# Performance work log

Hardware: AMD Instinct MI355X
Metric: run time of the kernel (lower is better)

The kernel has to match this reference:

```python
import jax, jax.numpy as jnp
import numpy as np

B, T, D, H = 2, 2048, 1024, 16  # batch, seq, hidden, heads; head_dim = 64


def setup_inputs() -> dict:
    key = jax.random.key(0)
    k1, k2, k3 = jax.random.split(key, 3)
    X = jax.random.normal(k1, (B, T, D), dtype=jnp.float32)
    # Dense(3*hidden_dim, use_bias=False): kernel [D, 3D]
    Wqkv = jax.random.normal(k2, (D, 3 * D), dtype=jnp.float32) / np.float32(np.sqrt(D))
    # Dense(hidden_dim, use_bias=False): kernel [D, D]
    Wproj = jax.random.normal(k3, (D, D), dtype=jnp.float32) / np.float32(np.sqrt(D))
    return {"X": X, "Wqkv": Wqkv, "Wproj": Wproj, "train": 0}


def reference(X, Wqkv, Wproj, train):
    # train=0 -> dropout is identity; the chunked online-softmax in the
    # original is mathematically exact softmax causal attention.
    b, t, d = X.shape
    hd = d // H
    qkv = X @ Wqkv                      # [B,T,3D]
    q, k, v = jnp.split(qkv, 3, axis=-1)
    q = q.reshape(b, t, H, hd)
    k = k.reshape(b, t, H, hd)
    v = v.reshape(b, t, H, hd)
    scale = 1.0 / jnp.sqrt(jnp.asarray(hd, dtype=X.dtype))
    scores = jnp.einsum('bqhd,bkhd->bhqk', q * scale, k)  # [B,H,T,T]
    causal = jnp.tril(jnp.ones((t, t), dtype=bool))
    scores = jnp.where(causal[None, None, :, :], scores, -jnp.inf)
    attn = jax.nn.softmax(scores, axis=-1)
    out = jnp.einsum('bhqk,bkhd->bqhd', attn, v).reshape(b, t, d)
    return out @ Wproj
```

## Files before the change

kernel.cpp:

```cpp
#include <hip/hip_runtime.h>


using u16 = unsigned short;
using u32 = unsigned int;

typedef __bf16 bf16x8 __attribute__((ext_vector_type(8)));
typedef __bf16 bf16x2 __attribute__((ext_vector_type(2)));
typedef float f32x4 __attribute__((ext_vector_type(4)));

#define DEV __device__ __forceinline__

DEV u16 f2bf(float f) { __bf16 h = (__bf16)f; return *(u16*)&h; }

DEV float bf2f(u16 v) {
  union { u32 u; float f; } x; x.u = (u32)v << 16; return x.f;
}

DEV u32 pk2(float lo, float hi) {
  bf16x2 t = {(__bf16)lo, (__bf16)hi};
  return *(u32*)&t;
}

DEV f32x4 mfma16(bf16x8 a, bf16x8 b, f32x4 c) {
  return __builtin_amdgcn_mfma_f32_16x16x32_bf16(a, b, c, 0, 0, 0);
}

DEV void gload_lds16(const void* g, void* l) {
  __builtin_amdgcn_global_load_lds(
      (const __attribute__((address_space(1))) void*)g,
      (__attribute__((address_space(3))) void*)l, 16, 0, 0);
}

DEV bf16x8 ld16(const u16* p) { return *(const bf16x8*)p; }

DEV void BAR() {
  __builtin_amdgcn_s_barrier();
  __builtin_amdgcn_sched_barrier(0);
}

DEV int vperm(int slot) {
  return ((((slot >> 4) & 2) | ((slot >> 2) & 1)) << 4) + (((slot >> 3) & 3) << 2) + (slot & 3);
}
DEV int vperm_inv(int k) {
  return (k & 0x23) | ((k & 0x10) >> 2) | ((k & 0x0c) << 1);
}


__global__ __launch_bounds__(256) void prep_kernel(
    const float* __restrict__ X, u16* __restrict__ Xb,
    const float* __restrict__ Wqkv, u16* __restrict__ Wqkvt,
    const float* __restrict__ Wproj, u16* __restrict__ Wprojt) {
  const int bid = blockIdx.x;
  const int t = threadIdx.x;

  if (bid < 2048) {
    int i = (bid * 256 + t) * 8;
    float4 a = *(const float4*)&X[i];
    float4 b = *(const float4*)&X[i + 4];
    union { u16 u[8]; uint4 v; } o;
    o.u[0] = f2bf(a.x); o.u[1] = f2bf(a.y); o.u[2] = f2bf(a.z); o.u[3] = f2bf(a.w);
    o.u[4] = f2bf(b.x); o.u[5] = f2bf(b.y); o.u[6] = f2bf(b.z); o.u[7] = f2bf(b.w);
    *(uint4*)&Xb[i] = o.v;
    return;
  }

  __shared__ float tile[64][65];
  const float* W; u16* Wt; int C, tb;
  if (bid < 2816) { W = Wqkv;  Wt = Wqkvt;  C = 3072; tb = bid - 2048; }
  else            { W = Wproj; Wt = Wprojt; C = 1024; tb = bid - 2816; }
  const int tilesC = C >> 6;
  const int tr = tb / tilesC, tc = tb % tilesC;
#pragma unroll
  for (int j = 0; j < 16; ++j) {
    int idx = j * 256 + t;
    int r = idx >> 6, c = idx & 63;
    tile[r][c] = W[(tr * 64 + r) * C + tc * 64 + c];
  }
  __syncthreads();
#pragma unroll
  for (int j = 0; j < 16; ++j) {
    int idx = j * 256 + t;
    int r = idx >> 6, c = idx & 63;
    Wt[(tc * 64 + r) * 1024 + tr * 64 + c] = f2bf(tile[c][r]);
  }
}


__global__ __launch_bounds__(512, 2) void gemm256_qkv_kernel(
    const u16* __restrict__ A, const u16* __restrict__ Bt,
    u16* __restrict__ Qb, u16* __restrict__ Kb, u16* __restrict__ VtP) {
  int bid = blockIdx.x;
  int bid2 = (bid & 7) * 32 + (bid >> 3);
  const int mt = bid2 >> 4, nt = bid2 & 15;
  const int m0 = mt * 256, n0 = nt * 192;
  const int tid = threadIdx.x;
  const int wid = tid >> 6, lane = tid & 63;
  const int g = lane >> 4, li = lane & 15;
  const int wm = wid >> 2, wn = wid & 3;

  __shared__ __align__(16) u16 lds[57344];

  const int srow = lane >> 3;
  const int scol = ((lane & 7) * 8) ^ ((srow & 7) << 3);

  auto ISSUE_A = [&](int s, int kt) {
    const int p = kt & 1;
#pragma unroll
    for (int is2 = 0; is2 < 2; ++is2) {
      int row = is2 * 64 + wid * 8 + srow;
      gload_lds16(&A[(size_t)(m0 + s * 128 + row) * 1024 + kt * 64 + scol],
                  &lds[s * 16384 + p * 8192 + is2 * 4096 + wid * 512]);
    }
  };
  auto ISSUE_B = [&](int kt) {
    const int p = kt & 1;
#pragma unroll
    for (int j = 0; j < 3; ++j) {
      int chunk = wid * 3 + j;
      int row = chunk * 8 + srow;
      gload_lds16(&Bt[(size_t)(n0 + row) * 1024 + kt * 64 + scol],
                  &lds[32768 + p * 12288 + chunk * 512]);
    }
  };

  auto LDA = [&](int p, int ks, bf16x8* aF) {
#pragma unroll
    for (int mi = 0; mi < 8; ++mi) {
      int row = mi * 16 + li;
      aF[mi] = ld16(&lds[wm * 16384 + p * 8192 + row * 64 +
                         ((ks * 32 + g * 8) ^ ((li & 7) << 3))]);
    }
  };
  auto LDB = [&](int p, int ks, bf16x8* bF) {
#pragma unroll
    for (int ni = 0; ni < 3; ++ni) {
      int row = wn * 48 + ni * 16 + li;
      bF[ni] = ld16(&lds[32768 + p * 12288 + row * 64 +
                         ((ks * 32 + g * 8) ^ ((li & 7) << 3))]);
    }
  };

  f32x4 acc[8][3] = {};
  bf16x8 a0[8], a1[8], bF[3];

  ISSUE_A(0, 0); ISSUE_A(1, 0); ISSUE_B(0);
  ISSUE_A(0, 1); ISSUE_A(1, 1);
  asm volatile("s_waitcnt vmcnt(4)" ::: "memory");
  BAR();

  for (int t = 0; t < 16; ++t) {
    const int p = t & 1;
    LDB(p, 0, bF);
    LDA(p, 0, a0);
    if (t + 1 < 16) ISSUE_B(t + 1);
    BAR();
    __builtin_amdgcn_s_setprio(1);
#pragma unroll
    for (int mi = 0; mi < 4; ++mi)
#pragma unroll
      for (int ni = 0; ni < 3; ++ni)
        acc[mi][ni] = mfma16(a0[mi], bF[ni], acc[mi][ni]);
    __builtin_amdgcn_s_setprio(0);
    BAR();
    LDA(p, 1, a1);
    BAR();
    __builtin_amdgcn_s_setprio(1);
#pragma unroll
    for (int mi = 4; mi < 8; ++mi)
#pragma unroll
      for (int ni = 0; ni < 3; ++ni)
        acc[mi][ni] = mfma16(a0[mi], bF[ni], acc[mi][ni]);
    __builtin_amdgcn_s_setprio(0);
    BAR();
    LDB(p, 1, bF);
    BAR();
    __builtin_amdgcn_s_setprio(1);
#pragma unroll
    for (int mi = 0; mi < 4; ++mi)
#pragma unroll
      for (int ni = 0; ni < 3; ++ni)
        acc[mi][ni] = mfma16(a1[mi], bF[ni], acc[mi][ni]);
    __builtin_amdgcn_s_setprio(0);
    BAR();
    if (t + 2 < 16) { ISSUE_A(0, t + 2); ISSUE_A(1, t + 2); }
    BAR();
    __builtin_amdgcn_s_setprio(1);
#pragma unroll
    for (int mi = 4; mi < 8; ++mi)
#pragma unroll
      for (int ni = 0; ni < 3; ++ni)
        acc[mi][ni] = mfma16(a1[mi], bF[ni], acc[mi][ni]);
    __builtin_amdgcn_s_setprio(0);
    if (t + 2 < 16) {
      asm volatile("s_waitcnt vmcnt(4)" ::: "memory");
    } else {
      asm volatile("s_waitcnt vmcnt(0)" ::: "memory");
    }
    BAR();
  }

#pragma unroll
  for (int mi = 0; mi < 8; ++mi)
#pragma unroll
    for (int ni = 0; ni < 3; ++ni) {
      int cc = n0 + wn * 48 + ni * 16 + li;
      int which = cc >> 10, rem = cc & 1023;
      int h = rem >> 6, dd = rem & 63;
      int rbase = m0 + wm * 128 + mi * 16 + g * 4;
      int bb = rbase >> 11, tt = rbase & 2047;
      if (which == 2) {
        int slot0 = (tt & ~63) + vperm_inv(tt & 63);
        size_t di = ((size_t)(bb * 16 + h) * 64 + dd) * 2048 + slot0;
        uint2 wv;
        wv.x = pk2(acc[mi][ni][0], acc[mi][ni][1]);
        wv.y = pk2(acc[mi][ni][2], acc[mi][ni][3]);
        *(uint2*)&VtP[di] = wv;
      } else {
        u16* dst = which == 0 ? Qb : Kb;
        float sc = which == 0 ? 0.18033688f : 1.0f;
        size_t di = ((size_t)(bb * 16 + h) * 2048 + tt) * 64 + dd;
#pragma unroll
        for (int r = 0; r < 4; ++r) dst[di + (size_t)r * 64] = f2bf(acc[mi][ni][r] * sc);
      }
    }
}


__global__ __launch_bounds__(256) void gemm_proj_kernel(
    const u16* __restrict__ A, const u16* __restrict__ Bt, float* __restrict__ OF) {
  int bid = blockIdx.x;
  int bid2 = (bid & 7) * 64 + (bid >> 3);
  const int mt = bid2 >> 3, nt = bid2 & 7;
  const int m0 = mt * 64, n0 = nt * 128;
  const int tid = threadIdx.x;
  const int wid = tid >> 6, lane = tid & 63;
  const int g = lane >> 4, li = lane & 15;
  const int wn = wid;

  __shared__ __align__(16) u16 As[2][64 * 64];
  __shared__ __align__(16) u16 Bs[2][128 * 64];

  f32x4 acc[4][2] = {};

  auto ISSUE = [&](int buf, int kt) {
#pragma unroll
    for (int iss = 0; iss < 2; ++iss) {
      int e = iss * 2048 + wid * 512 + lane * 8;
      int row = e >> 6;
      int kk = (e & 63) ^ ((row & 7) << 3);
      gload_lds16(&A[(size_t)(m0 + row) * 1024 + kt * 64 + kk], &As[buf][iss * 2048 + wid * 512]);
    }
#pragma unroll
    for (int iss = 0; iss < 4; ++iss) {
      int e = iss * 2048 + wid * 512 + lane * 8;
      int row = e >> 6;
      int kk = (e & 63) ^ ((row & 7) << 3);
      gload_lds16(&Bt[(size_t)(n0 + row) * 1024 + kt * 64 + kk], &Bs[buf][iss * 2048 + wid * 512]);
    }
  };

  ISSUE(0, 0);
  __syncthreads();
  int cur = 0;

  for (int kt = 0; kt < 16; ++kt) {
    if (kt + 1 < 16) ISSUE(cur ^ 1, kt + 1);
#pragma unroll
    for (int ks = 0; ks < 2; ++ks) {
      bf16x8 af[4], bfr[2];
#pragma unroll
      for (int mi = 0; mi < 4; ++mi)
        af[mi] = ld16(&As[cur][(mi * 16 + li) * 64 +
                               ((ks * 32 + g * 8) ^ ((li & 7) << 3))]);
#pragma unroll
      for (int ni = 0; ni < 2; ++ni)
        bfr[ni] = ld16(&Bs[cur][(wn * 32 + ni * 16 + li) * 64 +
                                ((ks * 32 + g * 8) ^ ((li & 7) << 3))]);
#pragma unroll
      for (int mi = 0; mi < 4; ++mi)
#pragma unroll
        for (int ni = 0; ni < 2; ++ni)
          acc[mi][ni] = mfma16(af[mi], bfr[ni], acc[mi][ni]);
    }
    __syncthreads();
    cur ^= 1;
  }

#pragma unroll
  for (int mi = 0; mi < 4; ++mi)
#pragma unroll
    for (int ni = 0; ni < 2; ++ni)
#pragma unroll
      for (int r = 0; r < 4; ++r) {
        int rr = m0 + mi * 16 + g * 4 + r;
        int cc = n0 + wn * 32 + ni * 16 + li;
        OF[(size_t)rr * 1024 + cc] = acc[mi][ni][r];
      }
}


__global__ __launch_bounds__(256) void attn_kernel(const u16* __restrict__ Q,
                                                   const u16* __restrict__ K,
                                                   const u16* __restrict__ VtP,
                                                   u16* __restrict__ AO,
                                                   u16* __restrict__ P2O,
                                                   float* __restrict__ L1,
                                                   float* __restrict__ L2) {
  const int bid = blockIdx.x;
  const int idx = bid >> 5;
  const int qt = 31 - (idx >> 1);
  const int half = idx & 1;
  const int bh = bid & 31;
  const int b = bh >> 4, h = bh & 15;
  const int tid = threadIdx.x;
  const int wid = tid >> 6, lane = tid & 63;
  const int g = lane >> 4, li = lane & 15;
  const int q0 = qt * 64;
  const int kmid = (qt + 2) >> 1;
  const int k0 = half ? kmid : 0;
  const int k1 = half ? qt + 1 : kmid;

  if (k0 >= k1) {
    if (tid < 64) L2[(size_t)bh * 2048 + q0 + tid] = 0.f;
    return;
  }

  __shared__ __align__(16) u16 Ks[2][64 * 64];
  __shared__ __align__(16) u16 Vs[2][64 * 64];

  const u16* Qh = Q + (size_t)bh * 2048 * 64;
  const u16* Kh = K + (size_t)bh * 2048 * 64;
  const u16* Vh = VtP + (size_t)bh * 64 * 2048;

  const int qrow = q0 + wid * 16 + li;
  bf16x8 qf[2];
#pragma unroll
  for (int ks = 0; ks < 2; ++ks)
    qf[ks] = ld16(&Qh[(size_t)qrow * 64 + ks * 32 + g * 8]);

  f32x4 accO[4] = {};
  f32x4 accL = {};
  union { u32 u[4]; bf16x8 v; } ones;
  ones.u[0] = ones.u[1] = ones.u[2] = ones.u[3] = 0x3F803F80u;

  auto STAGE = [&](int buf, int ktile) {
#pragma unroll
    for (int iss = 0; iss < 2; ++iss) {
      int e = iss * 2048 + wid * 512 + lane * 8;
      int row = e >> 6;
      int c0 = (e & 63) ^ ((row & 7) << 3);
      gload_lds16(&Kh[(size_t)(ktile * 64 + row) * 64 + c0],
                  &Ks[buf][iss * 2048 + wid * 512]);
      gload_lds16(&Vh[(size_t)row * 2048 + ktile * 64 + c0],
                  &Vs[buf][iss * 2048 + wid * 512]);
    }
  };

  STAGE(0, k0);
  STAGE(1, k0 + 1);
  int cur = 0;

  for (int kt = k0; kt < k1; ++kt) {
    if (kt + 1 < k1) {
      asm volatile("s_waitcnt vmcnt(4)" ::: "memory");
    } else {
      asm volatile("s_waitcnt vmcnt(0)" ::: "memory");
    }
    BAR();

    f32x4 s[4];
#pragma unroll
    for (int ni = 0; ni < 4; ++ni) s[ni] = f32x4{0.f, 0.f, 0.f, 0.f};
#pragma unroll
    for (int ks = 0; ks < 2; ++ks) {
      bf16x8 kf[4];
#pragma unroll
      for (int ni = 0; ni < 4; ++ni)
        kf[ni] = ld16(&Ks[cur][(ni * 16 + li) * 64 + ((ks * 32 + g * 8) ^ ((li & 7) << 3))]);
#pragma unroll
      for (int ni = 0; ni < 4; ++ni) s[ni] = mfma16(kf[ni], qf[ks], s[ni]);
    }

    if (kt == qt) {
      int ql = wid * 16 + li;
#pragma unroll
      for (int ni = 0; ni < 4; ++ni)
#pragma unroll
        for (int r = 0; r < 4; ++r)
          if (ni * 16 + g * 4 + r > ql) s[ni][r] = -1e30f;
    }

#pragma unroll
    for (int ni = 0; ni < 4; ++ni)
#pragma unroll
      for (int r = 0; r < 4; ++r) s[ni][r] = exp2f(s[ni][r]);

    union { u32 u[4]; bf16x8 v; } pf0, pf1;
    pf0.u[0] = pk2(s[0][0], s[0][1]); pf0.u[1] = pk2(s[0][2], s[0][3]);
    pf0.u[2] = pk2(s[1][0], s[1][1]); pf0.u[3] = pk2(s[1][2], s[1][3]);
    pf1.u[0] = pk2(s[2][0], s[2][1]); pf1.u[1] = pk2(s[2][2], s[2][3]);
    pf1.u[2] = pk2(s[3][0], s[3][1]); pf1.u[3] = pk2(s[3][2], s[3][3]);

    accL = mfma16(ones.v, pf0.v, accL);
    accL = mfma16(ones.v, pf1.v, accL);

#pragma unroll
    for (int ks = 0; ks < 2; ++ks) {
      bf16x8 pf = ks ? pf1.v : pf0.v;
#pragma unroll
      for (int mi = 0; mi < 4; ++mi) {
        bf16x8 vf = ld16(&Vs[cur][(mi * 16 + li) * 64 + ((ks * 32 + g * 8) ^ ((li & 7) << 3))]);
        accO[mi] = mfma16(vf, pf, accO[mi]);
      }
    }

    asm volatile("s_waitcnt lgkmcnt(0)" ::: "memory");
    BAR();
    if (kt + 2 < k1) STAGE(cur, kt + 2);
    cur ^= 1;
  }

  if (g == 0) (half ? L2 : L1)[(size_t)bh * 2048 + qrow] = accL[0];
  __syncthreads();
  u16* E = (u16*)Ks;
  int erow = wid * 16 + li;
#pragma unroll
  for (int mi = 0; mi < 4; ++mi) {
    uint2 wv;
    wv.x = pk2(accO[mi][0], accO[mi][1]);
    wv.y = pk2(accO[mi][2], accO[mi][3]);
    *(uint2*)&E[erow * 64 + ((mi * 16 + g * 4) ^ ((li & 7) << 3))] = wv;
  }
  __syncthreads();
#pragma unroll
  for (int pass = 0; pass < 2; ++pass) {
    int idx2 = pass * 2048 + tid * 8;
    int row = idx2 >> 6, col = idx2 & 63;
    uint4 val = *(uint4*)&E[row * 64 + (col ^ ((row & 7) << 3))];
    if (half == 0)
      *(uint4*)&AO[(size_t)(b * 2048 + q0 + row) * 1024 + h * 64 + col] = val;
    else
      *(uint4*)&P2O[((size_t)bh * 2048 + q0 + row) * 64 + col] = val;
  }
}

__global__ __launch_bounds__(256) void combine_kernel(u16* __restrict__ AO,
                                                      const u16* __restrict__ P2O,
                                                      const float* __restrict__ L1,
                                                      const float* __restrict__ L2) {
  int gid = blockIdx.x * 256 + threadIdx.x;
  int row = gid >> 3, dp = (gid & 7) * 8;
  int bh = row >> 11, q = row & 2047;
  int b = bh >> 4, h = bh & 15;
  float l2 = L2[row];
  float inv = 1.0f / (L1[row] + l2);
  float w2 = (l2 == 0.f) ? 0.f : inv;
  u16* ao = &AO[(size_t)(b * 2048 + q) * 1024 + h * 64 + dp];
  const u16* p2 = &P2O[(size_t)row * 64 + dp];
  union { uint4 v; u16 u[8]; } o1, o2, w;
  o1.v = *(const uint4*)ao;
  o2.v = *(const uint4*)p2;
#pragma unroll
  for (int j = 0; j < 8; ++j)
    w.u[j] = f2bf(bf2f(o1.u[j]) * inv + bf2f(o2.u[j]) * w2);
  *(uint4*)ao = w.v;
}


extern "C" void kernel_launch(void* const* d_in, const int* in_sizes, int n_in,
                              void* d_out, int out_size, void* d_ws, size_t ws_size,
                              hipStream_t stream) {
  const float* X = (const float*)d_in[0];
  const float* Wqkv = (const float*)d_in[1];
  const float* Wproj = (const float*)d_in[2];
  float* out = (float*)d_out;

  u16* ws = (u16*)d_ws;
  u16* Xb = ws;
  u16* Wqkvt = Xb + 4194304;
  u16* Wprojt = Wqkvt + 3145728;
  u16* Qb = Wprojt + 1048576;
  u16* Kb = Qb + 4194304;
  u16* VtP = Kb + 4194304;
  u16* AO = VtP + 4194304;
  u16* P2O = Xb;
  float* L1 = (float*)Wqkvt;
  float* L2 = L1 + 65536;

  prep_kernel<<<3072, 256, 0, stream>>>(X, Xb, Wqkv, Wqkvt, Wproj, Wprojt);
  gemm256_qkv_kernel<<<256, 512, 0, stream>>>(Xb, Wqkvt, Qb, Kb, VtP);
  attn_kernel<<<2048, 256, 0, stream>>>(Qb, Kb, VtP, AO, P2O, L1, L2);
  combine_kernel<<<2048, 256, 0, stream>>>(AO, P2O, L1, L2);
  gemm_proj_kernel<<<512, 256, 0, stream>>>(AO, Wprojt, out);
}
```

Before: 101.7 us.

## Fuse split-attention combine into projection GEMM A-tile loading

Removes the separate combine kernel that merged the two partial attention outputs, and does that merge inside the projection GEMM as its A tiles are loaded. A tiles now go through registers: the partial outputs and the L1/L2 sums are loaded, normalized and written swizzled into LDS, instead of using direct global-to-LDS loads. This saves one launch and one read-modify-write pass over AO. In exchange, each of the 8 N-tile blocks repeats the combine work and extra register-held loads stay in flight across the MFMA loop.

```diff
diff --git a/kernel.cpp b/kernel.cpp
--- a/kernel.cpp
+++ b/kernel.cpp
@@ -227,7 +227,9 @@
 
 
 __global__ __launch_bounds__(256) void gemm_proj_kernel(
-    const u16* __restrict__ A, const u16* __restrict__ Bt, float* __restrict__ OF) {
+    const u16* __restrict__ AO, const u16* __restrict__ P2O,
+    const float* __restrict__ L1, const float* __restrict__ L2,
+    const u16* __restrict__ Bt, float* __restrict__ OF) {
   int bid = blockIdx.x;
   int bid2 = (bid & 7) * 64 + (bid >> 3);
   const int mt = bid2 >> 3, nt = bid2 & 7;
@@ -242,14 +244,45 @@
 
   f32x4 acc[4][2] = {};
 
-  auto ISSUE = [&](int buf, int kt) {
+  int rowA[2], ddA[2];
+  float invA[2], w2A[2];
+  size_t prowA[2];
+#pragma unroll
+  for (int iss = 0; iss < 2; ++iss) {
+    int e = iss * 2048 + wid * 512 + lane * 8;
+    rowA[iss] = e >> 6;
+    ddA[iss] = e & 63;
+  }
+
+  union { uint4 v; u16 u[8]; } o1[2], o2[2];
+
+  auto ALOAD = [&](int kt) {
 #pragma unroll
     for (int iss = 0; iss < 2; ++iss) {
-      int e = iss * 2048 + wid * 512 + lane * 8;
-      int row = e >> 6;
-      int kk = (e & 63) ^ ((row & 7) << 3);
-      gload_lds16(&A[(size_t)(m0 + row) * 1024 + kt * 64 + kk], &As[buf][iss * 2048 + wid * 512]);
-    }
+      int rr = m0 + rowA[iss];
+      int bb = rr >> 11, tt = rr & 2047;
+      size_t prow = (size_t)(bb * 16 + kt) * 2048 + tt;
+      prowA[iss] = prow;
+      o1[iss].v = *(const uint4*)&AO[(size_t)rr * 1024 + kt * 64 + ddA[iss]];
+      o2[iss].v = *(const uint4*)&P2O[prow * 64 + ddA[iss]];
+      float l2v = L2[prow];
+      float inv = 1.0f / (L1[prow] + l2v);
+      invA[iss] = inv;
+      w2A[iss] = (l2v == 0.f) ? 0.f : inv;
+    }
+  };
+  auto AWRITE = [&](int buf) {
+#pragma unroll
+    for (int iss = 0; iss < 2; ++iss) {
+      union { uint4 v; u16 u[8]; } w;
+#pragma unroll
+      for (int j = 0; j < 8; ++j)
+        w.u[j] = f2bf(bf2f(o1[iss].u[j]) * invA[iss] + bf2f(o2[iss].u[j]) * w2A[iss]);
+      int dsw = ddA[iss] ^ ((rowA[iss] & 7) << 3);
+      *(uint4*)&As[buf][rowA[iss] * 64 + dsw] = w.v;
+    }
+  };
+  auto ISSUE_B = [&](int buf, int kt) {
 #pragma unroll
     for (int iss = 0; iss < 4; ++iss) {
       int e = iss * 2048 + wid * 512 + lane * 8;
@@ -259,12 +292,17 @@
     }
   };
 
-  ISSUE(0, 0);
+  ALOAD(0);
+  ISSUE_B(0, 0);
+  AWRITE(0);
   __syncthreads();
   int cur = 0;
 
   for (int kt = 0; kt < 16; ++kt) {
-    if (kt + 1 < 16) ISSUE(cur ^ 1, kt + 1);
+    if (kt + 1 < 16) {
+      ALOAD(kt + 1);
+      ISSUE_B(cur ^ 1, kt + 1);
+    }
 #pragma unroll
     for (int ks = 0; ks < 2; ++ks) {
       bf16x8 af[4], bfr[2];
@@ -282,6 +320,7 @@
         for (int ni = 0; ni < 2; ++ni)
           acc[mi][ni] = mfma16(af[mi], bfr[ni], acc[mi][ni]);
     }
+    if (kt + 1 < 16) AWRITE(cur ^ 1);
     __syncthreads();
     cur ^= 1;
   }
@@ -444,28 +483,6 @@
   }
 }
 
-__global__ __launch_bounds__(256) void combine_kernel(u16* __restrict__ AO,
-                                                      const u16* __restrict__ P2O,
-                                                      const float* __restrict__ L1,
-                                                      const float* __restrict__ L2) {
-  int gid = blockIdx.x * 256 + threadIdx.x;
-  int row = gid >> 3, dp = (gid & 7) * 8;
-  int bh = row >> 11, q = row & 2047;
-  int b = bh >> 4, h = bh & 15;
-  float l2 = L2[row];
-  float inv = 1.0f / (L1[row] + l2);
-  float w2 = (l2 == 0.f) ? 0.f : inv;
-  u16* ao = &AO[(size_t)(b * 2048 + q) * 1024 + h * 64 + dp];
-  const u16* p2 = &P2O[(size_t)row * 64 + dp];
-  union { uint4 v; u16 u[8]; } o1, o2, w;
-  o1.v = *(const uint4*)ao;
-  o2.v = *(const uint4*)p2;
-#pragma unroll
-  for (int j = 0; j < 8; ++j)
-    w.u[j] = f2bf(bf2f(o1.u[j]) * inv + bf2f(o2.u[j]) * w2);
-  *(uint4*)ao = w.v;
-}
-
 
 extern "C" void kernel_launch(void* const* d_in, const int* in_sizes, int n_in,
                               void* d_out, int out_size, void* d_ws, size_t ws_size,
@@ -490,6 +507,5 @@
   prep_kernel<<<3072, 256, 0, stream>>>(X, Xb, Wqkv, Wqkvt, Wproj, Wprojt);
   gemm256_qkv_kernel<<<256, 512, 0, stream>>>(Xb, Wqkvt, Qb, Kb, VtP);
   attn_kernel<<<2048, 256, 0, stream>>>(Qb, Kb, VtP, AO, P2O, L1, L2);
-  combine_kernel<<<2048, 256, 0, stream>>>(AO, P2O, L1, L2);
-  gemm_proj_kernel<<<512, 256, 0, stream>>>(AO, Wprojt, out);
-}
+  gemm_proj_kernel<<<512, 256, 0, stream>>>(AO, P2O, L1, L2, Wprojt, out);
+}
```

Result: no change. 103.1 us (+1.4%).
